# Kernel tuning notes

Measured on AMD Instinct MI355X. Metric: run time of the kernel, lower is better.

The kernel has to match this reference:

```python
import jax, jax.numpy as jnp
import numpy as np

ALPHA = 0.2  # LeakyReLU negative slope
EPS = 1e-8


def setup_inputs() -> dict:
    key = jax.random.key(0)
    ks = jax.random.split(key, 7)
    N, Fin, Fout, E = 100000, 256, 128, 800000
    node_embedding = jax.random.normal(ks[0], (N, Fin), dtype=jnp.float32)
    adj_pos = jax.random.randint(ks[1], (2, E), 0, N, dtype=jnp.int64)
    adj_neg = jax.random.randint(ks[2], (2, E), 0, N, dtype=jnp.int64)
    edge_embedding = jax.random.normal(ks[3], (2, Fout), dtype=jnp.float32)
    Wr = jax.random.normal(ks[4], (2, Fin, Fout), dtype=jnp.float32) * 0.05
    a = jax.random.normal(ks[5], (1, 2 * Fout), dtype=jnp.float32) * 0.05
    bias = jax.random.normal(ks[6], (1, Fout), dtype=jnp.float32) * 0.05
    return dict(node_embedding=node_embedding, edge_embedding=edge_embedding,
                Wr=Wr, a=a, bias=bias, adj_pos=adj_pos, adj_neg=adj_neg)


def reference(node_embedding, edge_embedding, Wr, a, bias, adj_pos, adj_neg):
    N = node_embedding.shape[0]
    Fout = Wr.shape[2]
    # h_r = X @ Wr[r], then column-scale by edge_embedding[r] (== mm with diag)
    h_pos = (node_embedding @ Wr[0]) * edge_embedding[0]  # [N, Fout]
    h_neg = (node_embedding @ Wr[1]) * edge_embedding[1]  # [N, Fout]
    a_src = a[0, :Fout]  # attention weights for source half of concat
    a_dst = a[0, Fout:]  # attention weights for dest half

    def edge_scores(h, adj):
        # a . [h[src], h[dst]] computed as node-level dots then scalar gather
        s = h @ a_src  # [N]
        d = h @ a_dst  # [N]
        z = s[adj[0]] + d[adj[1]]  # [E]
        z = jnp.where(z > 0, z, ALPHA * z)  # LeakyReLU
        return jax.nn.sigmoid(z)

    e_pos = edge_scores(h_pos, adj_pos)  # [E_pos]
    e_neg = edge_scores(h_neg, adj_neg)  # [E_neg]

    # row-sum normalizer: spmm(edge, edge_e, ones) == segment_sum over row idx
    rows = jnp.concatenate([adj_pos[0], adj_neg[0]])
    e_all = jnp.concatenate([e_pos, e_neg])
    row_sum = jax.ops.segment_sum(e_all, rows, num_segments=N) + EPS  # [N]

    # weighted aggregation: out[i] = sum_{(i,j)} e_ij * h[j]
    agg = (jax.ops.segment_sum(e_pos[:, None] * h_pos[adj_pos[1]], adj_pos[0], num_segments=N)
           + jax.ops.segment_sum(e_neg[:, None] * h_neg[adj_neg[1]], adj_neg[0], num_segments=N))
    return agg / row_sum[:, None] + bias
```

## Files before the change

### kernel.cpp

```cpp
#include <hip/hip_runtime.h>

#define ALPHA 0.2f
#define EPSV 1e-8f
#define BUCK_BITS 8
#define BUCK (1 << BUCK_BITS)
#define CAP 5120
#define EPB_A 4096
#define EPT_A (EPB_A / 256)

typedef float f32x4 __attribute__((ext_vector_type(4)));
typedef short bf16x8 __attribute__((ext_vector_type(8)));

static __device__ __forceinline__ unsigned short f2bf(float f) {
    union { float f; unsigned int u; } c; c.f = f;
    unsigned int u = c.u;
    unsigned int round = ((u >> 16) & 1) + 0x7FFF;
    return (unsigned short)((u + round) >> 16);
}
static __device__ __forceinline__ float bflo(unsigned int u) {
    union { unsigned int u; float f; } c; c.u = u << 16; return c.f;
}
static __device__ __forceinline__ float bfhi(unsigned int u) {
    union { unsigned int u; float f; } c; c.u = u & 0xFFFF0000u; return c.f;
}

__global__ __launch_bounds__(256) void convB_binA_kernel(
    const float* __restrict__ Wr, uint4* __restrict__ Bp,
    const int* __restrict__ adj_pos, const int* __restrict__ adj_neg,
    int* __restrict__ bucketCount, unsigned int* __restrict__ edges_tmp,
    int N, int E)
{
    __shared__ int hist[512];
    __shared__ int base[512];
    __shared__ int cur[512];
    const int tid = threadIdx.x;

    if ((int)blockIdx.x < 32) {
        const int t = blockIdx.x * 256 + tid;
        const int kb  = t >> 8;
        const int col = t & 255;
        const int rel = col >> 7;
        const int cc  = col & 127;
        unsigned short v[8];
        #pragma unroll
        for (int jj = 0; jj < 8; ++jj) {
            const int k = kb * 8 + jj;
            v[jj] = f2bf(Wr[(size_t)rel * 256 * 128 + (size_t)k * 128 + cc]);
        }
        Bp[t] = *reinterpret_cast<const uint4*>(v);
        return;
    }

    const int bb = blockIdx.x - 32;
    const long long e0 = (long long)bb * EPB_A;
    const long long twoE = 2LL * E;

    hist[tid] = 0;
    hist[tid + 256] = 0;

    int esrc[EPT_A];
    unsigned int erec[EPT_A];
    #pragma unroll
    for (int k = 0; k < EPT_A; ++k) {
        const long long idx = e0 + (long long)k * 256 + tid;
        if (idx < twoE) {
            const int rel = (idx >= E) ? 1 : 0;
            const long long eidx = rel ? idx - E : idx;
            const int* __restrict__ adj = rel ? adj_neg : adj_pos;
            const int src = adj[eidx];
            const int dst = adj[E + eidx];
            esrc[k] = src;
            erec[k] = (unsigned int)dst | ((unsigned int)rel << 17) |
                      ((unsigned int)(src & (BUCK - 1)) << 18);
        } else {
            esrc[k] = -1;
        }
    }
    __syncthreads();

    #pragma unroll
    for (int k = 0; k < EPT_A; ++k)
        if (esrc[k] >= 0) atomicAdd(&hist[esrc[k] >> BUCK_BITS], 1);
    __syncthreads();

    {
        const int rot = (bb * 61) & 511;
        #pragma unroll
        for (int q = 0; q < 2; ++q) {
            const int t2 = (tid + q * 256 + rot) & 511;
            const int hv = hist[t2];
            base[t2] = hv ? atomicAdd(&bucketCount[t2], hv) : 0;
            cur[t2] = 0;
        }
    }
    __syncthreads();

    #pragma unroll
    for (int k = 0; k < EPT_A; ++k) {
        if (esrc[k] >= 0) {
            const int b = esrc[k] >> BUCK_BITS;
            const int r = atomicAdd(&cur[b], 1);
            const int pos = base[b] + r;
            if (pos < CAP)
                edges_tmp[(size_t)b * CAP + pos] = erec[k];
        }
    }
}

__global__ __launch_bounds__(256) void mfma_gemm_kernel(
    const float* __restrict__ X, const uint4* __restrict__ Bp,
    const float* __restrict__ ee, const float* __restrict__ a,
    unsigned short* __restrict__ h, float* __restrict__ sd, int N)
{
    __shared__ unsigned short Alds[64 * 256];
    const int tid  = threadIdx.x;
    const int lane = tid & 63;
    const int w    = tid >> 6;
    const int wm   = w >> 1;
    const int wn   = w & 1;
    const int cl   = lane & 15;
    const int g    = lane >> 4;
    const int tile0 = blockIdx.x * 64;

    #pragma unroll
    for (int pass = 0; pass < 8; ++pass) {
        const int L  = pass * 256 + tid;
        const int r  = L >> 5;
        const int c8 = L & 31;
        const int row = tile0 + r;
        float4 f0 = make_float4(0.f, 0.f, 0.f, 0.f);
        float4 f1 = make_float4(0.f, 0.f, 0.f, 0.f);
        if (row < N) {
            const float* xp = &X[(size_t)row * 256 + c8 * 8];
            f0 = *reinterpret_cast<const float4*>(xp);
            f1 = *reinterpret_cast<const float4*>(xp + 4);
        }
        unsigned short v[8];
        v[0]=f2bf(f0.x); v[1]=f2bf(f0.y); v[2]=f2bf(f0.z); v[3]=f2bf(f0.w);
        v[4]=f2bf(f1.x); v[5]=f2bf(f1.y); v[6]=f2bf(f1.z); v[7]=f2bf(f1.w);
        const int su = c8 ^ (r & 7);
        *reinterpret_cast<bf16x8*>(&Alds[r * 256 + su * 8]) =
            *reinterpret_cast<const bf16x8*>(v);
    }
    __syncthreads();

    f32x4 acc[2][8];
    #pragma unroll
    for (int p = 0; p < 2; ++p)
        #pragma unroll
        for (int ct = 0; ct < 8; ++ct)
            acc[p][ct] = (f32x4){0.f, 0.f, 0.f, 0.f};

    const int rl0 = wm * 32 + cl;
    const int rl1 = rl0 + 16;
    #pragma unroll
    for (int kc = 0; kc < 8; ++kc) {
        const int ku = kc * 4 + g;
        const bf16x8 af0 = *reinterpret_cast<const bf16x8*>(
            &Alds[rl0 * 256 + (ku ^ (rl0 & 7)) * 8]);
        const bf16x8 af1 = *reinterpret_cast<const bf16x8*>(
            &Alds[rl1 * 256 + (ku ^ (rl1 & 7)) * 8]);
        bf16x8 bfr[8];
        #pragma unroll
        for (int ct = 0; ct < 8; ++ct) {
            const int col = wn * 128 + ct * 16 + cl;
            bfr[ct] = *reinterpret_cast<const bf16x8*>(Bp + ku * 256 + col);
        }
        #pragma unroll
        for (int ct = 0; ct < 8; ++ct)
            acc[0][ct] = __builtin_amdgcn_mfma_f32_16x16x32_bf16(
                af0, bfr[ct], acc[0][ct], 0, 0, 0);
        #pragma unroll
        for (int ct = 0; ct < 8; ++ct)
            acc[1][ct] = __builtin_amdgcn_mfma_f32_16x16x32_bf16(
                af1, bfr[ct], acc[1][ct], 0, 0, 0);
    }

    float eev[8], asv[8], adv[8];
    #pragma unroll
    for (int ct = 0; ct < 8; ++ct) {
        const int col = wn * 128 + ct * 16 + cl;
        const int cc  = col & 127;
        eev[ct] = ee[col];
        asv[ct] = a[cc];
        adv[ct] = a[128 + cc];
    }

    float s_acc[2][4], d_acc[2][4];
    #pragma unroll
    for (int p = 0; p < 2; ++p) {
        #pragma unroll
        for (int reg = 0; reg < 4; ++reg) {
            const int row = tile0 + wm * 32 + p * 16 + g * 4 + reg;
            const bool ok = row < N;
            float sp = 0.f, dp = 0.f;
            #pragma unroll
            for (int ct = 0; ct < 8; ++ct) {
                const float v = acc[p][ct][reg] * eev[ct];
                sp += v * asv[ct];
                dp += v * adv[ct];
                if (ok) {
                    const int cc = ct * 16 + cl;
                    h[((size_t)wn * N + row) * 128 + cc] = f2bf(v);
                }
            }
            s_acc[p][reg] = sp;
            d_acc[p][reg] = dp;
        }
    }
    #pragma unroll
    for (int p = 0; p < 2; ++p)
        #pragma unroll
        for (int reg = 0; reg < 4; ++reg) {
            float sp = s_acc[p][reg], dp = d_acc[p][reg];
            #pragma unroll
            for (int off = 1; off < 16; off <<= 1) {
                sp += __shfl_xor(sp, off);
                dp += __shfl_xor(dp, off);
            }
            if (cl == 0) {
                const int row = tile0 + wm * 32 + p * 16 + g * 4 + reg;
                if (row < N) {
                    sd[(size_t)wn * 2 * N + row]     = sp;
                    sd[(size_t)wn * 2 * N + N + row] = dp;
                }
            }
        }
}

__global__ __launch_bounds__(512) void sortB_kernel(
    const int* __restrict__ bucketCount, const unsigned int* __restrict__ edges_tmp,
    const float* __restrict__ sd,
    uint2* __restrict__ edges_final,
    int* __restrict__ rowBeg, int* __restrict__ rowEnd,
    float* __restrict__ rowSum, int N)
{
    __shared__ int hist[BUCK];
    __shared__ int cur[BUCK];
    __shared__ int ssum[BUCK];
    __shared__ float sSrc[2][BUCK];
    __shared__ float rsLds[BUCK];
    const int tid = threadIdx.x;
    const int b   = blockIdx.x;
    const int s0  = b << BUCK_BITS;
    const size_t tb = (size_t)b * CAP;
    const int cnt = min(bucketCount[b], CAP);

    if (tid < BUCK) {
        hist[tid] = 0;
        rsLds[tid] = 0.f;
        const int gsrc = s0 + tid;
        sSrc[0][tid] = (gsrc < N) ? sd[gsrc] : 0.f;
        sSrc[1][tid] = (gsrc < N) ? sd[2 * (size_t)N + gsrc] : 0.f;
    }
    __syncthreads();
    for (int j = tid; j < cnt; j += 512)
        atomicAdd(&hist[edges_tmp[tb + j] >> 18], 1);
    __syncthreads();

    int h0 = 0, incl = 0;
    if (tid < BUCK) { h0 = hist[tid]; ssum[tid] = h0; incl = h0; }
    __syncthreads();
    for (int off = 1; off < BUCK; off <<= 1) {
        const int u = (tid < BUCK && tid >= off) ? ssum[tid - off] : 0;
        __syncthreads();
        if (tid < BUCK) { incl += u; ssum[tid] = incl; }
        __syncthreads();
    }
    if (tid < BUCK) {
        const int excl = incl - h0;
        cur[tid] = excl;
        const int gidx = s0 + tid;
        if (gidx < N) {
            rowBeg[gidx] = (int)tb + excl;
            rowEnd[gidx] = (int)tb + incl;
        }
    }
    __syncthreads();
    for (int j = tid; j < cnt; j += 512) {
        const unsigned int r = edges_tmp[tb + j];
        const int sl  = r >> 18;
        const int rel = (r >> 17) & 1;
        const int dst = r & 0x1FFFF;
        float z = sSrc[rel][sl] + sd[(size_t)rel * 2 * N + N + dst];
        z = z > 0.f ? z : ALPHA * z;
        const float ev = 1.f / (1.f + __expf(-z));
        const int pos = atomicAdd(&cur[sl], 1);
        atomicAdd(&rsLds[sl], ev);
        edges_final[tb + pos] =
            make_uint2((unsigned int)(rel * N + dst), __float_as_uint(ev));
    }
    __syncthreads();
    if (tid < BUCK) {
        const int gidx = s0 + tid;
        if (gidx < N) rowSum[gidx] = rsLds[tid];
    }
}

__global__ __launch_bounds__(256) void gather_kernel(
    const int* __restrict__ rowBeg, const int* __restrict__ rowEnd,
    const float* __restrict__ rowSum,
    const uint2* __restrict__ edges,
    const unsigned short* __restrict__ h,
    const float* __restrict__ bias, float* __restrict__ out, int N)
{
    const long long gw = ((long long)blockIdx.x * blockDim.x + threadIdx.x) >> 6;
    const int lane = threadIdx.x & 63;
    if (gw >= N) return;
    const int n = (int)gw;

    const int beg = rowBeg[n];
    const int end = rowEnd[n];
    const unsigned loff = (unsigned)(lane << 2);
    const char* __restrict__ hb = (const char*)h;

    float ax = 0.f, ay = 0.f;
    int j = beg;
    for (; j + 8 <= end; j += 8) {
        uint2 r[8];
        #pragma unroll
        for (int k = 0; k < 8; ++k) r[k] = edges[j + k];
        unsigned int hv[8];
        #pragma unroll
        for (int k = 0; k < 8; ++k)
            hv[k] = *reinterpret_cast<const unsigned int*>(
                hb + ((r[k].x << 8) + loff));
        #pragma unroll
        for (int k = 0; k < 8; ++k) {
            const float e = __uint_as_float(r[k].y);
            ax += e * bflo(hv[k]);
            ay += e * bfhi(hv[k]);
        }
    }
    for (; j + 4 <= end; j += 4) {
        uint2 r[4];
        #pragma unroll
        for (int k = 0; k < 4; ++k) r[k] = edges[j + k];
        unsigned int hv[4];
        #pragma unroll
        for (int k = 0; k < 4; ++k)
            hv[k] = *reinterpret_cast<const unsigned int*>(
                hb + ((r[k].x << 8) + loff));
        #pragma unroll
        for (int k = 0; k < 4; ++k) {
            const float e = __uint_as_float(r[k].y);
            ax += e * bflo(hv[k]);
            ay += e * bfhi(hv[k]);
        }
    }
    for (; j < end; ++j) {
        const uint2 r = edges[j];
        const unsigned int hv = *reinterpret_cast<const unsigned int*>(
            hb + ((r.x << 8) + loff));
        const float e = __uint_as_float(r.y);
        ax += e * bflo(hv);
        ay += e * bfhi(hv);
    }
    const float inv = 1.f / (rowSum[n] + EPSV);
    const float2 bv = *reinterpret_cast<const float2*>(&bias[lane * 2]);
    float2 o;
    o.x = ax * inv + bv.x;
    o.y = ay * inv + bv.y;
    *reinterpret_cast<float2*>(&out[(size_t)n * 128 + lane * 2]) = o;
}

extern "C" void kernel_launch(void* const* d_in, const int* in_sizes, int n_in,
                              void* d_out, int out_size, void* d_ws, size_t ws_size,
                              hipStream_t stream) {
    const float* X      = (const float*)d_in[0];
    const float* ee     = (const float*)d_in[1];
    const float* Wr     = (const float*)d_in[2];
    const float* a      = (const float*)d_in[3];
    const float* bias   = (const float*)d_in[4];
    const int* adj_pos  = (const int*)d_in[5];
    const int* adj_neg  = (const int*)d_in[6];

    const int N = in_sizes[0] / 256;
    const int E = in_sizes[5] / 2;
    const int twoE = 2 * E;
    float* out = (float*)d_out;

    const int gemmBlocks = (N + 63) / 64;
    const int NBUCK = (N + BUCK - 1) >> BUCK_BITS;
    const int binBlocks = (twoE + EPB_A - 1) / EPB_A;

    char* ws = (char*)d_ws;
    uint4* Bp = (uint4*)ws;
    char* p = ws + 32 * 256 * 16;
    unsigned short* h = (unsigned short*)p; p += (size_t)2 * N * 128 * 2;
    float* sd         = (float*)p;  p += (size_t)4 * N * 4;
    int* bucketCount  = (int*)p;    p += 512 * 4;
    int* rowBeg       = (int*)p;    p += (size_t)N * 4;
    int* rowEnd       = (int*)p;    p += (size_t)N * 4;
    float* rowSum     = (float*)p;  p += (size_t)N * 4;
    p = (char*)(((uintptr_t)p + 15) & ~(uintptr_t)15);
    unsigned int* edges_tmp = (unsigned int*)p; p += (size_t)NBUCK * CAP * 4;
    uint2* edges_final = (uint2*)p; p += (size_t)NBUCK * CAP * 8;

    (void)hipMemsetAsync(bucketCount, 0, 512 * sizeof(int), stream);

    convB_binA_kernel<<<32 + binBlocks, 256, 0, stream>>>(
        Wr, Bp, adj_pos, adj_neg, bucketCount, edges_tmp, N, E);

    mfma_gemm_kernel<<<gemmBlocks, 256, 0, stream>>>(X, Bp, ee, a, h, sd, N);

    sortB_kernel<<<NBUCK, 512, 0, stream>>>(
        bucketCount, edges_tmp, sd, edges_final, rowBeg, rowEnd, rowSum, N);

    gather_kernel<<<(int)(((long long)N * 64 + 255) / 256), 256, 0, stream>>>(
        rowBeg, rowEnd, rowSum, edges_final, (const unsigned short*)h, bias, out, N);
}
```

Measured before the change: 175.3 us.

## Pre-convert X to bf16 MFMA fragment layout in prep kernel, stream fragments in GEMM

The fp32-to-bf16 conversion of X moves out of the GEMM into the prep kernel. That kernel writes a fragment-packed bf16 copy into the output buffer as scratch, in parallel with edge binning. The GEMM then loads A fragments straight from global memory with no LDS staging or barrier. In exchange there is an extra bf16 round trip of X through memory (write, then reread), plus a larger LDS footprint for the binning blocks.

After: 192.5 us. 9.8% more time.

```diff
diff --git a/kernel.cpp b/kernel.cpp
--- a/kernel.cpp
+++ b/kernel.cpp
@@ -24,19 +24,79 @@
     union { unsigned int u; float f; } c; c.u = u & 0xFFFF0000u; return c.f;
 }
 
-__global__ __launch_bounds__(256) void convB_binA_kernel(
+__global__ __launch_bounds__(256) void prep_kernel(
+    const float* __restrict__ X, uint4* __restrict__ Ap,
     const float* __restrict__ Wr, uint4* __restrict__ Bp,
     const int* __restrict__ adj_pos, const int* __restrict__ adj_neg,
     int* __restrict__ bucketCount, unsigned int* __restrict__ edges_tmp,
-    int N, int E)
+    int N, int E, int binBlocks)
 {
-    __shared__ int hist[512];
-    __shared__ int base[512];
-    __shared__ int cur[512];
+    __shared__ char smem[64 * 256 * 2];
     const int tid = threadIdx.x;
 
-    if ((int)blockIdx.x < 32) {
-        const int t = blockIdx.x * 256 + tid;
+    if ((int)blockIdx.x < binBlocks) {
+        int* hist = (int*)smem;
+        int* base = hist + 512;
+        int* cur  = base + 512;
+        const int bb = blockIdx.x;
+        const long long e0 = (long long)bb * EPB_A;
+        const long long twoE = 2LL * E;
+
+        hist[tid] = 0;
+        hist[tid + 256] = 0;
+
+        int esrc[EPT_A];
+        unsigned int erec[EPT_A];
+        #pragma unroll
+        for (int k = 0; k < EPT_A; ++k) {
+            const long long idx = e0 + (long long)k * 256 + tid;
+            if (idx < twoE) {
+                const int rel = (idx >= E) ? 1 : 0;
+                const long long eidx = rel ? idx - E : idx;
+                const int* __restrict__ adj = rel ? adj_neg : adj_pos;
+                const int src = adj[eidx];
+                const int dst = adj[E + eidx];
+                esrc[k] = src;
+                erec[k] = (unsigned int)dst | ((unsigned int)rel << 17) |
+                          ((unsigned int)(src & (BUCK - 1)) << 18);
+            } else {
+                esrc[k] = -1;
+            }
+        }
+        __syncthreads();
+
+        #pragma unroll
+        for (int k = 0; k < EPT_A; ++k)
+            if (esrc[k] >= 0) atomicAdd(&hist[esrc[k] >> BUCK_BITS], 1);
+        __syncthreads();
+
+        {
+            const int rot = (bb * 61) & 511;
+            #pragma unroll
+            for (int q = 0; q < 2; ++q) {
+                const int t2 = (tid + q * 256 + rot) & 511;
+                const int hv = hist[t2];
+                base[t2] = hv ? atomicAdd(&bucketCount[t2], hv) : 0;
+                cur[t2] = 0;
+            }
+        }
+        __syncthreads();
+
+        #pragma unroll
+        for (int k = 0; k < EPT_A; ++k) {
+            if (esrc[k] >= 0) {
+                const int b = esrc[k] >> BUCK_BITS;
+                const int r = atomicAdd(&cur[b], 1);
+                const int pos = base[b] + r;
+                if (pos < CAP)
+                    edges_tmp[(size_t)b * CAP + pos] = erec[k];
+            }
+        }
+        return;
+    }
+
+    if ((int)blockIdx.x < binBlocks + 32) {
+        const int t = (blockIdx.x - binBlocks) * 256 + tid;
         const int kb  = t >> 8;
         const int col = t & 255;
         const int rel = col >> 7;
@@ -51,98 +111,58 @@
         return;
     }
 
-    const int bb = blockIdx.x - 32;
-    const long long e0 = (long long)bb * EPB_A;
-    const long long twoE = 2LL * E;
-
-    hist[tid] = 0;
-    hist[tid + 256] = 0;
-
-    int esrc[EPT_A];
-    unsigned int erec[EPT_A];
-    #pragma unroll
-    for (int k = 0; k < EPT_A; ++k) {
-        const long long idx = e0 + (long long)k * 256 + tid;
-        if (idx < twoE) {
-            const int rel = (idx >= E) ? 1 : 0;
-            const long long eidx = rel ? idx - E : idx;
-            const int* __restrict__ adj = rel ? adj_neg : adj_pos;
-            const int src = adj[eidx];
-            const int dst = adj[E + eidx];
-            esrc[k] = src;
-            erec[k] = (unsigned int)dst | ((unsigned int)rel << 17) |
-                      ((unsigned int)(src & (BUCK - 1)) << 18);
-        } else {
-            esrc[k] = -1;
-        }
-    }
-    __syncthreads();
-
-    #pragma unroll
-    for (int k = 0; k < EPT_A; ++k)
-        if (esrc[k] >= 0) atomicAdd(&hist[esrc[k] >> BUCK_BITS], 1);
-    __syncthreads();
-
-    {
-        const int rot = (bb * 61) & 511;
-        #pragma unroll
-        for (int q = 0; q < 2; ++q) {
-            const int t2 = (tid + q * 256 + rot) & 511;
-            const int hv = hist[t2];
-            base[t2] = hv ? atomicAdd(&bucketCount[t2], hv) : 0;
-            cur[t2] = 0;
-        }
-    }
-    __syncthreads();
-
-    #pragma unroll
-    for (int k = 0; k < EPT_A; ++k) {
-        if (esrc[k] >= 0) {
-            const int b = esrc[k] >> BUCK_BITS;
-            const int r = atomicAdd(&cur[b], 1);
-            const int pos = base[b] + r;
-            if (pos < CAP)
-                edges_tmp[(size_t)b * CAP + pos] = erec[k];
+    unsigned short* T = (unsigned short*)smem;
+    const int cb = blockIdx.x - binBlocks - 32;
+    const int tile0 = cb * 64;
+    const float4* __restrict__ X4 = (const float4*)X;
+
+    #pragma unroll
+    for (int p = 0; p < 16; ++p) {
+        const int f  = p * 256 + tid;
+        const int r  = f >> 6;
+        const int c4 = f & 63;
+        const int row = tile0 + r;
+        float4 v4 = make_float4(0.f, 0.f, 0.f, 0.f);
+        if (row < N) v4 = X4[(size_t)row * 64 + c4];
+        unsigned short v[4];
+        v[0] = f2bf(v4.x); v[1] = f2bf(v4.y); v[2] = f2bf(v4.z); v[3] = f2bf(v4.w);
+        const int kbu  = c4 >> 1;
+        const int half = c4 & 1;
+        const int su   = kbu ^ (r & 7);
+        *reinterpret_cast<uint2*>(&T[r * 256 + su * 8 + half * 4]) =
+            *reinterpret_cast<const uint2*>(v);
+    }
+    __syncthreads();
+
+    #pragma unroll
+    for (int q = 0; q < 8; ++q) {
+        const int u    = q * 256 + tid;
+        const int rt_l = u >> 9;
+        const int kb   = (u >> 4) & 31;
+        const int i    = u & 15;
+        const int row_l = rt_l * 16 + i;
+        const int grow  = tile0 + row_l;
+        if (grow < N) {
+            const int su = kb ^ (row_l & 7);
+            Ap[((size_t)(tile0 >> 4) + rt_l) * 512 + (size_t)kb * 16 + i] =
+                *reinterpret_cast<const uint4*>(&T[row_l * 256 + su * 8]);
         }
     }
 }
 
 __global__ __launch_bounds__(256) void mfma_gemm_kernel(
-    const float* __restrict__ X, const uint4* __restrict__ Bp,
+    const uint4* __restrict__ Ap, const uint4* __restrict__ Bp,
     const float* __restrict__ ee, const float* __restrict__ a,
     unsigned short* __restrict__ h, float* __restrict__ sd, int N)
 {
-    __shared__ unsigned short Alds[64 * 256];
     const int tid  = threadIdx.x;
     const int lane = tid & 63;
     const int w    = tid >> 6;
     const int wm   = w >> 1;
     const int wn   = w & 1;
+    const int rtb  = blockIdx.x * 4 + wm * 2;
     const int cl   = lane & 15;
     const int g    = lane >> 4;
-    const int tile0 = blockIdx.x * 64;
-
-    #pragma unroll
-    for (int pass = 0; pass < 8; ++pass) {
-        const int L  = pass * 256 + tid;
-        const int r  = L >> 5;
-        const int c8 = L & 31;
-        const int row = tile0 + r;
-        float4 f0 = make_float4(0.f, 0.f, 0.f, 0.f);
-        float4 f1 = make_float4(0.f, 0.f, 0.f, 0.f);
-        if (row < N) {
-            const float* xp = &X[(size_t)row * 256 + c8 * 8];
-            f0 = *reinterpret_cast<const float4*>(xp);
-            f1 = *reinterpret_cast<const float4*>(xp + 4);
-        }
-        unsigned short v[8];
-        v[0]=f2bf(f0.x); v[1]=f2bf(f0.y); v[2]=f2bf(f0.z); v[3]=f2bf(f0.w);
-        v[4]=f2bf(f1.x); v[5]=f2bf(f1.y); v[6]=f2bf(f1.z); v[7]=f2bf(f1.w);
-        const int su = c8 ^ (r & 7);
-        *reinterpret_cast<bf16x8*>(&Alds[r * 256 + su * 8]) =
-            *reinterpret_cast<const bf16x8*>(v);
-    }
-    __syncthreads();
 
     f32x4 acc[2][8];
     #pragma unroll
@@ -151,29 +171,31 @@
         for (int ct = 0; ct < 8; ++ct)
             acc[p][ct] = (f32x4){0.f, 0.f, 0.f, 0.f};
 
-    const int rl0 = wm * 32 + cl;
-    const int rl1 = rl0 + 16;
+    const bool ld0 = (rtb + 1) * 16 <= N;
+    const bool ld1 = (rtb + 2) * 16 <= N;
+    const bf16x8 zf = (bf16x8){0,0,0,0,0,0,0,0};
+
     #pragma unroll
     for (int kc = 0; kc < 8; ++kc) {
-        const int ku = kc * 4 + g;
-        const bf16x8 af0 = *reinterpret_cast<const bf16x8*>(
-            &Alds[rl0 * 256 + (ku ^ (rl0 & 7)) * 8]);
-        const bf16x8 af1 = *reinterpret_cast<const bf16x8*>(
-            &Alds[rl1 * 256 + (ku ^ (rl1 & 7)) * 8]);
-        bf16x8 bfr[8];
+        bf16x8 af[2], bfr[8];
+        af[0] = ld0 ? *reinterpret_cast<const bf16x8*>(
+            Ap + ((size_t)rtb * 32 + kc * 4) * 16 + lane) : zf;
+        af[1] = ld1 ? *reinterpret_cast<const bf16x8*>(
+            Ap + ((size_t)(rtb + 1) * 32 + kc * 4) * 16 + lane) : zf;
         #pragma unroll
         for (int ct = 0; ct < 8; ++ct) {
+            const int kb  = kc * 4 + g;
             const int col = wn * 128 + ct * 16 + cl;
-            bfr[ct] = *reinterpret_cast<const bf16x8*>(Bp + ku * 256 + col);
+            bfr[ct] = *reinterpret_cast<const bf16x8*>(Bp + kb * 256 + col);
         }
         #pragma unroll
         for (int ct = 0; ct < 8; ++ct)
             acc[0][ct] = __builtin_amdgcn_mfma_f32_16x16x32_bf16(
-                af0, bfr[ct], acc[0][ct], 0, 0, 0);
+                af[0], bfr[ct], acc[0][ct], 0, 0, 0);
         #pragma unroll
         for (int ct = 0; ct < 8; ++ct)
             acc[1][ct] = __builtin_amdgcn_mfma_f32_16x16x32_bf16(
-                af1, bfr[ct], acc[1][ct], 0, 0, 0);
+                af[1], bfr[ct], acc[1][ct], 0, 0, 0);
     }
 
     float eev[8], asv[8], adv[8];
@@ -191,7 +213,7 @@
     for (int p = 0; p < 2; ++p) {
         #pragma unroll
         for (int reg = 0; reg < 4; ++reg) {
-            const int row = tile0 + wm * 32 + p * 16 + g * 4 + reg;
+            const int row = (rtb + p) * 16 + g * 4 + reg;
             const bool ok = row < N;
             float sp = 0.f, dp = 0.f;
             #pragma unroll
@@ -219,7 +241,7 @@
                 dp += __shfl_xor(dp, off);
             }
             if (cl == 0) {
-                const int row = tile0 + wm * 32 + p * 16 + g * 4 + reg;
+                const int row = (rtb + p) * 16 + g * 4 + reg;
                 if (row < N) {
                     sd[(size_t)wn * 2 * N + row]     = sp;
                     sd[(size_t)wn * 2 * N + N + row] = dp;
@@ -382,7 +404,10 @@
 
     const int gemmBlocks = (N + 63) / 64;
     const int NBUCK = (N + BUCK - 1) >> BUCK_BITS;
-    const int binBlocks = (twoE + EPB_A - 1) / EPB_A;
+    const int binBlocks  = (twoE + EPB_A - 1) / EPB_A;
+    const int convBlocks = (N + 63) / 64;
+
+    uint4* Ap = (uint4*)d_out;
 
     char* ws = (char*)d_ws;
     uint4* Bp = (uint4*)ws;
@@ -399,10 +424,10 @@
 
     (void)hipMemsetAsync(bucketCount, 0, 512 * sizeof(int), stream);
 
-    convB_binA_kernel<<<32 + binBlocks, 256, 0, stream>>>(
-        Wr, Bp, adj_pos, adj_neg, bucketCount, edges_tmp, N, E);
-
-    mfma_gemm_kernel<<<gemmBlocks, 256, 0, stream>>>(X, Bp, ee, a, h, sd, N);
+    prep_kernel<<<binBlocks + 32 + convBlocks, 256, 0, stream>>>(
+        X, Ap, Wr, Bp, adj_pos, adj_neg, bucketCount, edges_tmp, N, E, binBlocks);
+
+    mfma_gemm_kernel<<<gemmBlocks, 256, 0, stream>>>(Ap, Bp, ee, a, h, sd, N);
 
     sortB_kernel<<<NBUCK, 512, 0, stream>>>(
         bucketCount, edges_tmp, sd, edges_final, rowBeg, rowEnd, rowSum, N);
```
